# Performance work log

Measured on AMD Instinct MI355X. Metric: run time of the kernel, lower is better.

The kernel has to match this reference:

```python
import jax, jax.numpy as jnp
import numpy as np

N_NODES = 50000
N_EDGES = 800000
H_DIM = 128
N_REL = 40
N_BASES = 4


def setup_inputs() -> dict:
    key = jax.random.key(0)
    ks = jax.random.split(key, 9)
    h = jax.random.normal(ks[0], (N_NODES, H_DIM), jnp.float32)
    norm = jax.random.uniform(ks[1], (N_EDGES, 1), jnp.float32)
    basis_w = jax.random.normal(ks[2], (N_BASES, H_DIM, H_DIM), jnp.float32) * 0.05
    w_comp = jax.random.normal(ks[3], (N_REL, N_BASES), jnp.float32) * 0.5
    loop_w = jax.random.normal(ks[4], (H_DIM, H_DIM), jnp.float32) * 0.05
    bias = jax.random.normal(ks[5], (H_DIM,), jnp.float32) * 0.05
    src = jax.random.randint(ks[6], (N_EDGES,), 0, N_NODES, jnp.int32)
    dst = jax.random.randint(ks[7], (N_EDGES,), 0, N_NODES, jnp.int32)
    etype = jax.random.randint(ks[8], (N_EDGES,), 0, N_REL, jnp.int32)
    return {"h": h, "norm": norm, "basis_w": basis_w, "w_comp": w_comp,
            "loop_w": loop_w, "bias": bias, "src": src, "dst": dst, "etype": etype}


def reference(h, norm, basis_w, w_comp, loop_w, bias, src, dst, etype):
    # RelGraphConv with 'basis' regularizer, one layer (num_hidden_layers=1):
    #   W_r = sum_b w_comp[r, b] * basis_w[b]
    #   m_e = (h[src_e] @ W_{etype_e}) * norm_e
    #   agg[v] = sum_{e: dst_e = v} m_e
    #   out = relu(agg + bias + h @ loop_w)   (dropout = 0)
    # Contraction reordered for memory efficiency: scatter-add per-basis
    # scaled source features first (node-level), then apply small basis GEMMs.
    n = h.shape[0]
    n_bases = basis_w.shape[0]
    coeff = w_comp[etype] * norm          # [E, B] per-edge basis coefficients * norm
    h_src = h[src]                        # [E, D] edge-gathered source features
    agg = jnp.zeros((n, basis_w.shape[2]), dtype=h.dtype)
    for b in range(n_bases):              # small fixed loop over bases
        s_b = jax.ops.segment_sum(coeff[:, b:b + 1] * h_src, dst, num_segments=n)  # [N, D]
        agg = agg + s_b @ basis_w[b]
    return jax.nn.relu(agg + bias + h @ loop_w)
```

## Files before the change

### kernel.cpp

```cpp
#include <hip/hip_runtime.h>
#include <stdint.h>

#define N_NODES 50000
#define N_EDGES 800000
#define H_DIM 128
#define N_REL 40
#define N_BASES 4
#define N_RANGES 196
#define EP_BLOCKS 400
#define EDGES_PER_BLK 2000
#define STAGE_CAP 5120
#define CAST_BLOCKS 1563

typedef __attribute__((ext_vector_type(8))) short bf16x8;
typedef __attribute__((ext_vector_type(4))) float f32x4;

__device__ __forceinline__ unsigned short f2bf(float f) {
    unsigned int u = __float_as_uint(f);
    unsigned int r = u + 0x7fffu + ((u >> 16) & 1u);
    return (unsigned short)(r >> 16);
}

__global__ __launch_bounds__(1024) void edge_pack(
        const int* __restrict__ src, const int* __restrict__ dst,
        const int* __restrict__ etype, const float* __restrict__ norm,
        uint2* __restrict__ pkd, int* __restrict__ gcnt,
        unsigned* __restrict__ sorted_src, float4* __restrict__ sorted_cf) {
    __shared__ int lhist[N_RANGES];
    int blk = blockIdx.x;
    int t = threadIdx.x;
    if (t < N_RANGES) lhist[t] = 0;
    if (blk == 0 && t >= 1008) {
        int k = t - 1008;
        sorted_src[N_EDGES + k] = 0u;
        sorted_cf[N_EDGES + k] = make_float4(0.f, 0.f, 0.f, 0.f);
    }
    __syncthreads();
    int e0 = blk * EDGES_PER_BLK;
    for (int i = t; i < EDGES_PER_BLK; i += 1024) {
        int e = e0 + i;
        int d = dst[e];
        unsigned int nbf = f2bf(norm[e]);
        pkd[e] = make_uint2((unsigned)src[e] | ((unsigned)etype[e] << 20),
                            (unsigned)d | (nbf << 17));
        atomicAdd(&lhist[d >> 8], 1);
    }
    __syncthreads();
    if (t < N_RANGES) gcnt[blk * N_RANGES + t] = lhist[t];
}

__global__ __launch_bounds__(512) void bucket_scan_a(
        const int* __restrict__ gcnt, int* __restrict__ blkbase,
        int* __restrict__ btot) {
    __shared__ int wsum[8];
    int r = blockIdx.x;
    int t = threadIdx.x, lane = t & 63, w = t >> 6;
    int x = (t < EP_BLOCKS) ? gcnt[t * N_RANGES + r] : 0;
    int v = x;
#pragma unroll
    for (int d = 1; d < 64; d <<= 1) {
        int y = __shfl_up(v, d);
        if (lane >= d) v += y;
    }
    if (lane == 63) wsum[w] = v;
    __syncthreads();
    int wpre = 0;
#pragma unroll
    for (int ww = 0; ww < 7; ++ww)
        if (w > ww) wpre += wsum[ww];
    if (t < EP_BLOCKS) blkbase[t * N_RANGES + r] = wpre + v - x;
    if (t == 511) btot[r] = wpre + v;
}

__global__ __launch_bounds__(512) void stage2(
        const float* __restrict__ h,
        const float* __restrict__ basis_w, const float* __restrict__ loop_w,
        const uint2* __restrict__ pkd, const int* __restrict__ blkbase,
        const int* __restrict__ btot,
        unsigned short* __restrict__ A, unsigned short* __restrict__ wt3,
        uint2* __restrict__ bucketed) {
    __shared__ int lcur[N_RANGES];
    __shared__ int wsum[8];
    int bid = blockIdx.x;
    int t = threadIdx.x;
    if (bid < EP_BLOCKS) {
        int lane = t & 63, w = t >> 6;
        int b = bid;
        int x = (t < N_RANGES) ? btot[t] : 0;
        int v = x;
#pragma unroll
        for (int d = 1; d < 64; d <<= 1) {
            int y = __shfl_up(v, d);
            if (lane >= d) v += y;
        }
        if (lane == 63) wsum[w] = v;
        __syncthreads();
        int wpre = 0;
#pragma unroll
        for (int ww = 0; ww < 7; ++ww)
            if (w > ww) wpre += wsum[ww];
        if (t < N_RANGES)
            lcur[t] = (wpre + v - x) + blkbase[b * N_RANGES + t];
        __syncthreads();
        int e0 = b * EDGES_PER_BLK;
        for (int i = t; i < EDGES_PER_BLK; i += 512) {
            uint2 p = pkd[e0 + i];
            int r = (p.y & 0x1FFFF) >> 8;
            int pos = atomicAdd(&lcur[r], 1);
            bucketed[pos] = p;
        }
    } else if (bid < EP_BLOCKS + CAST_BLOCKS) {
        int g = (bid - EP_BLOCKS) * 512 + t;
        if (g < 800000) {
            int row = g >> 4;
            int cb = (g & 15) * 8;
            const float* p = h + (size_t)row * 128 + cb;
            float4 a0 = ((const float4*)p)[0];
            float4 a1 = ((const float4*)p)[1];
            bf16x8 o;
            o[0] = (short)f2bf(a0.x); o[1] = (short)f2bf(a0.y);
            o[2] = (short)f2bf(a0.z); o[3] = (short)f2bf(a0.w);
            o[4] = (short)f2bf(a1.x); o[5] = (short)f2bf(a1.y);
            o[6] = (short)f2bf(a1.z); o[7] = (short)f2bf(a1.w);
            *(bf16x8*)(A + (size_t)row * H_DIM + cb) = o;
        }
    } else {
        int mat = bid - EP_BLOCKS - CAST_BLOCKS;
        const float* srcm = (mat < 4) ? (basis_w + mat * 16384) : loop_w;
        int koff = (mat < 4) ? (128 + mat * 128) : 0;
#pragma unroll
        for (int i = 0; i < 8; ++i) {
            int f = t + i * 512;
            int k = f >> 5;
            int j4 = (f & 31) * 4;
            float4 v = ((const float4*)srcm)[f];
            int kg = koff + k;
            int ks = kg >> 5;
            int quad = (kg >> 3) & 3;
            int jj = kg & 7;
            float vv[4] = {v.x, v.y, v.z, v.w};
#pragma unroll
            for (int d = 0; d < 4; ++d) {
                int j = j4 + d;
                int cg = j >> 4;
                int n16 = j & 15;
                wt3[(size_t)((ks * 8 + cg) * 64 + quad * 16 + n16) * 8 + jj] =
                    f2bf(vv[d]);
            }
        }
    }
}

__global__ __launch_bounds__(1024) void bucket_sort(
        const int* __restrict__ btot, const uint2* __restrict__ bucketed,
        const float* __restrict__ w_comp,
        unsigned* __restrict__ sorted_src, float4* __restrict__ sorted_cf,
        int* __restrict__ offs) {
    __shared__ int hist[256];
    __shared__ int cur[256];
    __shared__ int wsum[16];
    __shared__ int sbeg;
    __shared__ uint2 stage[STAGE_CAP];
    int r = blockIdx.x;
    int t = threadIdx.x, lane = t & 63, w = t >> 6;
    int x = (t < N_RANGES) ? btot[t] : 0;
    int v = x;
#pragma unroll
    for (int d = 1; d < 64; d <<= 1) {
        int y = __shfl_up(v, d);
        if (lane >= d) v += y;
    }
    if (lane == 63) wsum[w] = v;
    if (t < 256) hist[t] = 0;
    __syncthreads();
    int wpre = 0;
#pragma unroll
    for (int ww = 0; ww < 15; ++ww)
        if (w > ww) wpre += wsum[ww];
    if (t == r) sbeg = wpre + v - x;
    __syncthreads();
    int begin = sbeg;
    int n = btot[r];
    int end = begin + n;
    for (int i = begin + t; i < end; i += 1024)
        atomicAdd(&hist[bucketed[i].y & 255], 1);
    __syncthreads();
    int x2 = (t < 256) ? hist[t] : 0;
    int v2 = x2;
#pragma unroll
    for (int d = 1; d < 64; d <<= 1) {
        int y = __shfl_up(v2, d);
        if (lane >= d) v2 += y;
    }
    if (lane == 63) wsum[w] = v2;
    __syncthreads();
    if (t < 256) {
        int wpre2 = 0;
#pragma unroll
        for (int ww = 0; ww < 3; ++ww)
            if (w > ww) wpre2 += wsum[ww];
        int excl_rel = wpre2 + v2 - x2;
        int node = r * 256 + t;
        if (node < N_NODES) offs[node] = begin + excl_rel;
        cur[t] = excl_rel;
    }
    if (r == N_RANGES - 1 && t == 0) offs[N_NODES] = N_EDGES;
    __syncthreads();
    if (n <= STAGE_CAP) {
        for (int i = begin + t; i < end; i += 1024) {
            uint2 p = bucketed[i];
            int pos = atomicAdd(&cur[p.y & 255], 1);
            stage[pos] = make_uint2(p.x, (p.y >> 17) << 16);
        }
        __syncthreads();
        for (int i = t; i < n; i += 1024) {
            uint2 p = stage[i];
            float nm = __uint_as_float(p.y);
            float4 wc = ((const float4*)w_comp)[p.x >> 20];
            sorted_src[begin + i] = p.x & 0xFFFFF;
            sorted_cf[begin + i] =
                make_float4(wc.x * nm, wc.y * nm, wc.z * nm, wc.w * nm);
        }
    } else {
        for (int i = begin + t; i < end; i += 1024) {
            uint2 p = bucketed[i];
            int pos = atomicAdd(&cur[p.y & 255], 1);
            float nm = __uint_as_float((p.y >> 17) << 16);
            float4 wc = ((const float4*)w_comp)[p.x >> 20];
            sorted_src[begin + pos] = p.x & 0xFFFFF;
            sorted_cf[begin + pos] =
                make_float4(wc.x * nm, wc.y * nm, wc.z * nm, wc.w * nm);
        }
    }
}

__global__ __launch_bounds__(512, 8) void agg_gemm(
        const int* __restrict__ offs, const unsigned* __restrict__ ssrc,
        const float4* __restrict__ scf,
        const unsigned short* __restrict__ Ab,
        const unsigned short* __restrict__ wt3,
        const float* __restrict__ bias, float* __restrict__ out) {
    __shared__ __align__(16) unsigned short S[32 * 640];
    int wv = threadIdx.x >> 6;
    int lane = threadIdx.x & 63;
    int nbase = blockIdx.x * 32;
    const unsigned int* Au = (const unsigned int*)Ab;

#pragma unroll
    for (int q = 0; q < 4; ++q) {
        int row = (wv << 2) + q;
        int v = __builtin_amdgcn_readfirstlane(nbase + row);
        float a0l = 0.f, a0h = 0.f, a1l = 0.f, a1h = 0.f;
        float a2l = 0.f, a2h = 0.f, a3l = 0.f, a3h = 0.f;
        unsigned int hb = 0u;
        if (v < N_NODES) {
            hb = Au[(size_t)v * 64 + lane];
            int begin = __builtin_amdgcn_readfirstlane(offs[v]);
            int end   = __builtin_amdgcn_readfirstlane(offs[v + 1]);
            for (int j = begin; j < end; j += 8) {
                int rem = end - j;
                unsigned su[8];
                float4 c[8];
#pragma unroll
                for (int k = 0; k < 8; ++k) su[k] = ssrc[j + k];
#pragma unroll
                for (int k = 0; k < 8; ++k) c[k] = scf[j + k];
                if (rem < 8) {
#pragma unroll
                    for (int k = 0; k < 8; ++k)
                        if (k >= rem) {
                            su[k] = 0u;
                            c[k] = make_float4(0.f, 0.f, 0.f, 0.f);
                        }
                }
                unsigned u[8];
#pragma unroll
                for (int k = 0; k < 8; ++k)
                    u[k] = Au[(size_t)su[k] * 64 + lane];
#pragma unroll
                for (int k = 0; k < 8; ++k) {
                    float lo = __uint_as_float(u[k] << 16);
                    float hi = __uint_as_float(u[k] & 0xffff0000u);
                    a0l += c[k].x * lo; a0h += c[k].x * hi;
                    a1l += c[k].y * lo; a1h += c[k].y * hi;
                    a2l += c[k].z * lo; a2h += c[k].z * hi;
                    a3l += c[k].w * lo; a3h += c[k].w * hi;
                }
            }
        }
        char* rp = (char*)S + row * 1280;
        int swz = (row & 7) << 4;
        *(unsigned int*)(rp + ((lane * 4) ^ swz)) = hb;
        *(unsigned int*)(rp + ((256 + lane * 4) ^ swz)) =
            (unsigned int)f2bf(a0l) | ((unsigned int)f2bf(a0h) << 16);
        *(unsigned int*)(rp + ((512 + lane * 4) ^ swz)) =
            (unsigned int)f2bf(a1l) | ((unsigned int)f2bf(a1h) << 16);
        *(unsigned int*)(rp + ((768 + lane * 4) ^ swz)) =
            (unsigned int)f2bf(a2l) | ((unsigned int)f2bf(a2h) << 16);
        *(unsigned int*)(rp + ((1024 + lane * 4) ^ swz)) =
            (unsigned int)f2bf(a3l) | ((unsigned int)f2bf(a3h) << 16);
    }
    __syncthreads();

    int n16 = lane & 15;
    int quad = lane >> 4;
    f32x4 acc0 = (f32x4)0.f, acc1 = (f32x4)0.f;

    const char* s0p = (const char*)S + n16 * 1280;
    const char* s1p = s0p + 16 * 1280;
    int swz2 = (n16 & 7) << 4;
    const unsigned short* bwp = wt3 + (size_t)wv * 512 + (size_t)lane * 8;

#pragma unroll
    for (int ks = 0; ks < 20; ++ks) {
        int off = (ks * 64 + quad * 16) ^ swz2;
        bf16x8 a0 = *(const bf16x8*)(s0p + off);
        bf16x8 a1 = *(const bf16x8*)(s1p + off);
        bf16x8 b  = *(const bf16x8*)(bwp + (size_t)ks * 4096);
        acc0 = __builtin_amdgcn_mfma_f32_16x16x32_bf16(a0, b, acc0, 0, 0, 0);
        acc1 = __builtin_amdgcn_mfma_f32_16x16x32_bf16(a1, b, acc1, 0, 0, 0);
    }

    int col = (wv << 4) + n16;
    float bv = bias[col];
#pragma unroll
    for (int rg = 0; rg < 4; ++rg) {
        int r0 = nbase + quad * 4 + rg;
        if (r0 < N_NODES)
            out[(size_t)r0 * H_DIM + col] = fmaxf(acc0[rg] + bv, 0.f);
        int r1 = nbase + 16 + quad * 4 + rg;
        if (r1 < N_NODES)
            out[(size_t)r1 * H_DIM + col] = fmaxf(acc1[rg] + bv, 0.f);
    }
}

extern "C" void kernel_launch(void* const* d_in, const int* in_sizes, int n_in,
                              void* d_out, int out_size, void* d_ws, size_t ws_size,
                              hipStream_t stream) {
    const float* h       = (const float*)d_in[0];
    const float* norm    = (const float*)d_in[1];
    const float* basis_w = (const float*)d_in[2];
    const float* w_comp  = (const float*)d_in[3];
    const float* loop_w  = (const float*)d_in[4];
    const float* bias    = (const float*)d_in[5];
    const int*   src     = (const int*)d_in[6];
    const int*   dst     = (const int*)d_in[7];
    const int*   etype   = (const int*)d_in[8];
    float* out = (float*)d_out;

    char* base = (char*)d_ws;
    unsigned short* wt3       = (unsigned short*)(base + 0);
    unsigned short* A         = (unsigned short*)(base + 163840);
    int*            offs      = (int*)(base + 12963840);
    uint2*          pkd       = (uint2*)(base + 13163848);
    uint2*          bucketed  = (uint2*)(base + 19563848);
    float4*         sorted_cf = (float4*)(base + 25963856);
    unsigned*       sorted_src= (unsigned*)(base + 38764112);
    int*            gcnt      = (int*)(base + 41964176);
    int*            blkbase   = (int*)(base + 42277776);
    int*            btot      = (int*)(base + 42591376);

    edge_pack<<<EP_BLOCKS, 1024, 0, stream>>>(src, dst, etype, norm,
                                              pkd, gcnt,
                                              sorted_src, sorted_cf);
    bucket_scan_a<<<N_RANGES, 512, 0, stream>>>(gcnt, blkbase, btot);
    stage2<<<EP_BLOCKS + CAST_BLOCKS + 5, 512, 0, stream>>>(
        h, basis_w, loop_w, pkd, blkbase, btot, A, wt3, bucketed);
    bucket_sort<<<N_RANGES, 1024, 0, stream>>>(btot, bucketed, w_comp,
                                               sorted_src, sorted_cf, offs);
    agg_gemm<<<1563, 512, 0, stream>>>(offs, sorted_src, sorted_cf,
                                       A, wt3, bias, out);
}
```

Measured before the change: 166.5 us.

## Split bucket_sort across four sub-blocks per node range

Each node range is now handled by four 512-thread blocks instead of one 1024-thread block. Each block owns 64 of the 256 destination nodes, stages only its own edges in a smaller shared buffer and writes only its own slice of offsets and sorted outputs. The aim is more blocks to fill the GPU's compute units and less LDS per block, so more blocks can be resident at once. The cost is that every sub-block re-reads the whole bucket and rebuilds the full histogram, which quadruples that redundant work and its global reads.

```diff
diff --git a/kernel.cpp b/kernel.cpp
--- a/kernel.cpp
+++ b/kernel.cpp
@@ -9,7 +9,7 @@
 #define N_RANGES 196
 #define EP_BLOCKS 400
 #define EDGES_PER_BLK 2000
-#define STAGE_CAP 5120
+#define STAGE_CAP 2048
 #define CAST_BLOCKS 1563
 
 typedef __attribute__((ext_vector_type(8))) short bf16x8;
@@ -151,17 +151,19 @@
     }
 }
 
-__global__ __launch_bounds__(1024) void bucket_sort(
+__global__ __launch_bounds__(512) void bucket_sort(
         const int* __restrict__ btot, const uint2* __restrict__ bucketed,
         const float* __restrict__ w_comp,
         unsigned* __restrict__ sorted_src, float4* __restrict__ sorted_cf,
         int* __restrict__ offs) {
     __shared__ int hist[256];
     __shared__ int cur[256];
-    __shared__ int wsum[16];
+    __shared__ int wsum[8];
     __shared__ int sbeg;
     __shared__ uint2 stage[STAGE_CAP];
-    int r = blockIdx.x;
+    int bid = blockIdx.x;
+    int r = bid >> 2;
+    int sub = bid & 3;
     int t = threadIdx.x, lane = t & 63, w = t >> 6;
     int x = (t < N_RANGES) ? btot[t] : 0;
     int v = x;
@@ -175,14 +177,14 @@
     __syncthreads();
     int wpre = 0;
 #pragma unroll
-    for (int ww = 0; ww < 15; ++ww)
+    for (int ww = 0; ww < 7; ++ww)
         if (w > ww) wpre += wsum[ww];
     if (t == r) sbeg = wpre + v - x;
     __syncthreads();
     int begin = sbeg;
     int n = btot[r];
     int end = begin + n;
-    for (int i = begin + t; i < end; i += 1024)
+    for (int i = begin + t; i < end; i += 512)
         atomicAdd(&hist[bucketed[i].y & 255], 1);
     __syncthreads();
     int x2 = (t < 256) ? hist[t] : 0;
@@ -200,36 +202,48 @@
         for (int ww = 0; ww < 3; ++ww)
             if (w > ww) wpre2 += wsum[ww];
         int excl_rel = wpre2 + v2 - x2;
-        int node = r * 256 + t;
-        if (node < N_NODES) offs[node] = begin + excl_rel;
         cur[t] = excl_rel;
-    }
-    if (r == N_RANGES - 1 && t == 0) offs[N_NODES] = N_EDGES;
-    __syncthreads();
-    if (n <= STAGE_CAP) {
-        for (int i = begin + t; i < end; i += 1024) {
+        if ((t >> 6) == sub) {
+            int node = r * 256 + t;
+            if (node < N_NODES) offs[node] = begin + excl_rel;
+        }
+    }
+    if (r == N_RANGES - 1 && sub == 3 && t == 0) offs[N_NODES] = N_EDGES;
+    __syncthreads();
+    int lo = cur[sub * 64];
+    int hi_ = (sub == 3) ? n : cur[sub * 64 + 64];
+    int m = hi_ - lo;
+    __syncthreads();
+    if (m <= STAGE_CAP) {
+        for (int i = begin + t; i < end; i += 512) {
             uint2 p = bucketed[i];
-            int pos = atomicAdd(&cur[p.y & 255], 1);
-            stage[pos] = make_uint2(p.x, (p.y >> 17) << 16);
+            int d = p.y & 255;
+            if ((d >> 6) == sub) {
+                int pos = atomicAdd(&cur[d], 1);
+                stage[pos - lo] = make_uint2(p.x, (p.y >> 17) << 16);
+            }
         }
         __syncthreads();
-        for (int i = t; i < n; i += 1024) {
+        for (int i = t; i < m; i += 512) {
             uint2 p = stage[i];
             float nm = __uint_as_float(p.y);
             float4 wc = ((const float4*)w_comp)[p.x >> 20];
-            sorted_src[begin + i] = p.x & 0xFFFFF;
-            sorted_cf[begin + i] =
+            sorted_src[begin + lo + i] = p.x & 0xFFFFF;
+            sorted_cf[begin + lo + i] =
                 make_float4(wc.x * nm, wc.y * nm, wc.z * nm, wc.w * nm);
         }
     } else {
-        for (int i = begin + t; i < end; i += 1024) {
+        for (int i = begin + t; i < end; i += 512) {
             uint2 p = bucketed[i];
-            int pos = atomicAdd(&cur[p.y & 255], 1);
-            float nm = __uint_as_float((p.y >> 17) << 16);
-            float4 wc = ((const float4*)w_comp)[p.x >> 20];
-            sorted_src[begin + pos] = p.x & 0xFFFFF;
-            sorted_cf[begin + pos] =
-                make_float4(wc.x * nm, wc.y * nm, wc.z * nm, wc.w * nm);
+            int d = p.y & 255;
+            if ((d >> 6) == sub) {
+                int pos = atomicAdd(&cur[d], 1);
+                float nm = __uint_as_float((p.y >> 17) << 16);
+                float4 wc = ((const float4*)w_comp)[p.x >> 20];
+                sorted_src[begin + pos] = p.x & 0xFFFFF;
+                sorted_cf[begin + pos] =
+                    make_float4(wc.x * nm, wc.y * nm, wc.z * nm, wc.w * nm);
+            }
         }
     }
 }
@@ -366,8 +380,8 @@
     bucket_scan_a<<<N_RANGES, 512, 0, stream>>>(gcnt, blkbase, btot);
     stage2<<<EP_BLOCKS + CAST_BLOCKS + 5, 512, 0, stream>>>(
         h, basis_w, loop_w, pkd, blkbase, btot, A, wt3, bucketed);
-    bucket_sort<<<N_RANGES, 1024, 0, stream>>>(btot, bucketed, w_comp,
-                                               sorted_src, sorted_cf, offs);
+    bucket_sort<<<N_RANGES * 4, 512, 0, stream>>>(btot, bucketed, w_comp,
+                                                  sorted_src, sorted_cf, offs);
     agg_gemm<<<1563, 512, 0, stream>>>(offs, sorted_src, sorted_cf,
                                        A, wt3, bias, out);
 }
```

After: 170.0 us. 1.02x slower.
